# Kernel optimization log

Hardware: AMD Instinct MI355X
Metric: run time of the kernel (lower is better)

## Reference

```python
import jax, jax.numpy as jnp
import numpy as np

B, N, E = 32, 1024, 16384
IN_DIM, HID, OUT = 768, 512, 400
H, F = 2, 200          # gat heads, per-head dim (H*F == OUT)
PAIR = 2 * OUT         # 800
NEG_SLOPE = 0.2


def setup_inputs() -> dict:
    key = jax.random.key(0)
    ks = jax.random.split(key, 20)
    g = lambda k, shp, fan: jax.random.normal(k, shp, jnp.float32) * (1.0 / np.sqrt(fan))
    return {
        "patch_features": jax.random.normal(ks[0], (B, N, IN_DIM), jnp.float32),
        "edges": jax.random.randint(ks[1], (2, E), 0, N, jnp.int32),
        # patch_encoder Mlps: 768 -> 512 (GELU) -> 400
        "enc_w1": g(ks[2], (IN_DIM, HID), IN_DIM), "enc_b1": jnp.zeros((HID,), jnp.float32),
        "enc_w2": g(ks[3], (HID, OUT), HID),      "enc_b2": jnp.zeros((OUT,), jnp.float32),
        # single GATConv: 400 -> 2 heads x 200, concat
        "gat_w": g(ks[4], (OUT, H, F), OUT),
        "att_src": g(ks[5], (H, F), F), "att_dst": g(ks[6], (H, F), F),
        "gat_b": jnp.zeros((H * F,), jnp.float32),
        # predict_head Mlps: 800 -> 800 (GELU) -> 400 (GELU) -> 3
        "h_w1": g(ks[7], (PAIR, PAIR), PAIR),      "h_b1": jnp.zeros((PAIR,), jnp.float32),
        "h_w2": g(ks[8], (PAIR, PAIR // 2), PAIR), "h_b2": jnp.zeros((PAIR // 2,), jnp.float32),
        "h_w3": g(ks[9], (PAIR // 2, 3), PAIR // 2), "h_b3": jnp.zeros((3,), jnp.float32),
    }


def _forward(patch_features, edges, enc_w1, enc_b1, enc_w2, enc_b2,
             gat_w, att_src, att_dst, gat_b,
             h_w1, h_b1, h_w2, h_b2, h_w3, h_b3):
    n = patch_features.shape[1]
    # per-batch patch encoder MLP (dropout inactive at eval)
    enc = jax.nn.gelu(jnp.einsum('bni,ih->bnh', patch_features, enc_w1) + enc_b1)
    enc = jnp.einsum('bnh,ho->bno', enc, enc_w2) + enc_b2   # [B,N,400]

    src0, dst0 = edges[0], edges[1]
    # GATConv adds self-loops
    loops = jnp.arange(n, dtype=edges.dtype)
    src = jnp.concatenate([src0, loops])
    dst = jnp.concatenate([dst0, loops])

    def gat(h):                                   # h: [N,400]
        wh = jnp.einsum('no,ohf->nhf', h, gat_w)  # [N,H,F]
        a_s = jnp.sum(wh * att_src, -1)           # [N,H]
        a_d = jnp.sum(wh * att_dst, -1)
        e = a_s[src] + a_d[dst]                   # [Et,H]
        e = jnp.where(e > 0, e, NEG_SLOPE * e)    # LeakyReLU(0.2)
        m = jax.ops.segment_max(e, dst, num_segments=n)
        ee = jnp.exp(e - m[dst])
        z = jax.ops.segment_sum(ee, dst, num_segments=n)
        coef = ee / z[dst]                        # softmax over incoming edges
        out = jax.ops.segment_sum(coef[:, :, None] * wh[src], dst, num_segments=n)
        return out.reshape(n, H * F) + gat_b      # concat heads + bias

    feat = enc + jax.vmap(gat)(enc)               # residual add per batch

    # pairwise edge gather + predict head
    pair = jnp.concatenate([feat[:, src0], feat[:, dst0]], axis=-1)  # [B,E,800]
    p = jax.nn.gelu(jnp.einsum('bep,pq->beq', pair, h_w1) + h_b1)
    p = jax.nn.gelu(jnp.einsum('beq,qr->ber', p, h_w2) + h_b2)
    pred = jnp.einsum('ber,rs->bes', p, h_w3) + h_b3                 # [B,E,3]
    return feat, pred


def reference(patch_features, edges, enc_w1, enc_b1, enc_w2, enc_b2,
              gat_w, att_src, att_dst, gat_b,
              h_w1, h_b1, h_w2, h_b2, h_w3, h_b3):
    return _forward(patch_features, edges, enc_w1, enc_b1, enc_w2, enc_b2,
                    gat_w, att_src, att_dst, gat_b,
                    h_w1, h_b1, h_w2, h_b2, h_w3, h_b3)
```

## Files before the change

kernel.cpp:

```cpp
#include <hip/hip_runtime.h>
#include <hip/hip_bf16.h>

typedef unsigned short u16;
typedef __attribute__((ext_vector_type(8))) short bf16x8;
typedef __attribute__((ext_vector_type(4))) float f32x4;

#define B_   32
#define N_   1024
#define E_   16384
#define ET_  17408
#define IN_DIM 768
#define HID  512
#define OUT_ 400
#define PAIR_ 800
#define UVW_ 1600
#define FEAT_ELEMS 13107200
#define MAXD 128

__device__ __forceinline__ float u2f(u16 u) {
    union { unsigned int i; float f; } v; v.i = ((unsigned int)u) << 16; return v.f;
}
__device__ __forceinline__ u16 f2u(float f) {
    __hip_bfloat16 h = __float2bfloat16(f);
    return *(u16*)&h;
}
__device__ __forceinline__ unsigned int pack2(float a, float b) {
    return (unsigned int)f2u(a) | ((unsigned int)f2u(b) << 16);
}

__device__ __forceinline__ float gelu_f(float x) {
    const float c = 0.7978845608028654f;
    float u = c * (x + 0.044715f * x * x * x);
    float t = 2.0f / (1.0f + __expf(-2.0f * u)) - 1.0f;
    return 0.5f * x * (1.0f + t);
}

__device__ __forceinline__ void load_lds16(const void* g, void* l) {
    __builtin_amdgcn_global_load_lds(
        (const __attribute__((address_space(1))) void*)g,
        (__attribute__((address_space(3))) void*)l, 16, 0, 0);
}

__global__ void wt_k(const float* __restrict__ W, u16* __restrict__ Wt,
                     int K, int N)
{
    int i = blockIdx.x * 256 + threadIdx.x;
    if (i >= N * K) return;
    int n = i / K, k = i - n * K;
    Wt[i] = f2u(W[(size_t)k * N + n]);
}

__global__ void wtuv_k(const float* __restrict__ W, u16* __restrict__ Wt)
{
    int i = blockIdx.x * 256 + threadIdx.x;
    if (i >= UVW_ * OUT_) return;
    int n = i / OUT_, k = i - n * OUT_;
    int row = (n >= PAIR_) ? OUT_ + k : k;
    int col = (n >= PAIR_) ? n - PAIR_ : n;
    Wt[i] = f2u(W[(size_t)row * PAIR_ + col]);
}

__global__ void f2b_k(const float* __restrict__ X, u16* __restrict__ Y, int n8)
{
    int i = blockIdx.x * 256 + threadIdx.x;
    if (i >= n8) return;
    const float4* p = (const float4*)X + (size_t)i * 2;
    float4 a = p[0], b = p[1];
    uint4 o;
    o.x = pack2(a.x, a.y); o.y = pack2(a.z, a.w);
    o.z = pack2(b.x, b.y); o.w = pack2(b.z, b.w);
    ((uint4*)Y)[i] = o;
}

template<int ASRC, bool DO_GELU, bool HAS_BIAS, bool OUT_F32>
__global__ __launch_bounds__(256)
void mfma_gemm_k(const float* __restrict__ Af, const u16* __restrict__ Ab,
                 const u16* __restrict__ Wt, const float* __restrict__ bias,
                 u16* __restrict__ Cb, float* __restrict__ Cf,
                 int M, int N, int K,
                 const u16* __restrict__ zbuf)
{
    __shared__ __align__(16) u16 As[128 * 64];
    __shared__ __align__(16) u16 Bs[128 * 64];
    const int tid  = threadIdx.x;
    const int gx   = gridDim.x;
    const int nwg  = gx * gridDim.y;
    const int orig = blockIdx.y * gx + blockIdx.x;
    const int qc   = nwg >> 3, rc = nwg & 7;
    const int xcd  = orig & 7, lid = orig >> 3;
    const int wg   = ((xcd < rc) ? xcd * (qc + 1) : rc * (qc + 1) + (xcd - rc) * qc) + lid;
    const int bm   = (wg / gx) * 128;
    const int bn   = (wg % gx) * 128;
    const int wave = tid >> 6;
    const int lane = tid & 63;
    const int wm   = (wave >> 1) * 64;
    const int wn   = (wave & 1) * 64;
    const int lm   = lane & 15;
    const int lq   = lane >> 4;
    const int lb   = lm & 7;
    const int l8 = lane >> 3;
    const int cl = (lane & 7) ^ l8;

    size_t arow[4]; size_t brow[4]; bool bok[4];
    #pragma unroll
    for (int c4 = 0; c4 < 4; ++c4) {
        int rt = wave * 32 + c4 * 8 + l8;
        if (ASRC == 1) arow[c4] = (size_t)(bm + rt) * K;
        int n = bn + rt;
        bok[c4] = (n < N);
        brow[c4] = (size_t)(n < N ? n : 0) * K;
    }
    const int vrow = tid >> 1, vhalf = tid & 1;

    f32x4 acc[4][4] = {};

    for (int k0 = 0; k0 < K; k0 += 64) {
        if (ASRC == 1) {
            int kk = k0 + cl * 8;
            #pragma unroll
            for (int c4 = 0; c4 < 4; ++c4) {
                const u16* ga = (kk < K) ? Ab + arow[c4] + kk : zbuf;
                load_lds16(ga, (char*)As + (wave * 32 + c4 * 8) * 128);
            }
        } else {
            #pragma unroll
            for (int c = 0; c < 4; ++c) {
                int c_log = vhalf * 4 + c;
                int kk = k0 + c_log * 8;
                uint4 wv = make_uint4(0, 0, 0, 0);
                if (kk < K) {
                    const float* p = Af + (size_t)(bm + vrow) * K + kk;
                    float4 v0 = *(const float4*)p;
                    float4 v1 = *(const float4*)(p + 4);
                    wv.x = pack2(v0.x, v0.y); wv.y = pack2(v0.z, v0.w);
                    wv.z = pack2(v1.x, v1.y); wv.w = pack2(v1.z, v1.w);
                }
                int pc = c_log ^ (vrow & 7);
                *(uint4*)((char*)As + vrow * 128 + pc * 16) = wv;
            }
        }
        {
            int kk = k0 + cl * 8;
            #pragma unroll
            for (int c4 = 0; c4 < 4; ++c4) {
                const u16* gb = (bok[c4] && kk < K) ? Wt + brow[c4] + kk : zbuf;
                load_lds16(gb, (char*)Bs + (wave * 32 + c4 * 8) * 128);
            }
        }
        __syncthreads();
        #pragma unroll
        for (int kh = 0; kh < 2; ++kh) {
            bf16x8 af[4], bfr[4];
            #pragma unroll
            for (int t = 0; t < 4; ++t)
                af[t] = *(const bf16x8*)((const char*)As +
                        (wm + t * 16 + lm) * 128 + (((kh * 4 + lq) ^ lb) * 16));
            #pragma unroll
            for (int u = 0; u < 4; ++u)
                bfr[u] = *(const bf16x8*)((const char*)Bs +
                        (wn + u * 16 + lm) * 128 + (((kh * 4 + lq) ^ lb) * 16));
            #pragma unroll
            for (int t = 0; t < 4; ++t)
                #pragma unroll
                for (int u = 0; u < 4; ++u)
                    acc[t][u] = __builtin_amdgcn_mfma_f32_16x16x32_bf16(
                        af[t], bfr[u], acc[t][u], 0, 0, 0);
        }
        __syncthreads();
    }

    #pragma unroll
    for (int u = 0; u < 4; ++u) {
        int col = bn + wn + u * 16 + lm;
        if (col >= N) continue;
        float bv = HAS_BIAS ? bias[col] : 0.f;
        #pragma unroll
        for (int t = 0; t < 4; ++t) {
            #pragma unroll
            for (int r = 0; r < 4; ++r) {
                int rowg = bm + wm + t * 16 + lq * 4 + r;
                float v = acc[t][u][r] + bv;
                if (DO_GELU) v = gelu_f(v);
                if (OUT_F32) {
                    Cf[(size_t)rowg * N + col] = v;
                    if (Cb) Cb[(size_t)rowg * N + col] = f2u(v);
                } else {
                    Cb[(size_t)rowg * N + col] = f2u(v);
                }
            }
        }
    }
}

__global__ __launch_bounds__(256)
void pair_fuse_k(const u16* __restrict__ UV, const float* __restrict__ b1,
                 const int* __restrict__ src0, const int* __restrict__ dst0,
                 u16* __restrict__ p1, int b0, int nrows)
{
    int r  = blockIdx.x * 2 + (threadIdx.x >> 7);
    int c8 = threadIdx.x & 127;
    if (c8 >= 100 || r >= nrows) return;
    int e = r & (E_ - 1);
    int gs, gd;
    if (b0 >= 0) {
        int b = b0 + (r >> 14);
        gs = (b << 10) + src0[e];
        gd = (b << 10) + dst0[e];
    } else {
        gs = src0[e]; gd = dst0[e];
    }
    uint4 qu = *(const uint4*)(UV + (size_t)gs * UVW_ + c8 * 8);
    uint4 qv = *(const uint4*)(UV + (size_t)gd * UVW_ + PAIR_ + c8 * 8);
    float4 bva = *(const float4*)(b1 + c8 * 8);
    float4 bvb = *(const float4*)(b1 + c8 * 8 + 4);
    float bb[8] = {bva.x, bva.y, bva.z, bva.w, bvb.x, bvb.y, bvb.z, bvb.w};
    unsigned int uu[4] = {qu.x, qu.y, qu.z, qu.w};
    unsigned int vv[4] = {qv.x, qv.y, qv.z, qv.w};
    uint4 o; unsigned int* op = (unsigned int*)&o;
    #pragma unroll
    for (int q = 0; q < 4; ++q) {
        float a0 = u2f((u16)(uu[q] & 0xffff)) + u2f((u16)(vv[q] & 0xffff)) + bb[2*q];
        float a1 = u2f((u16)(uu[q] >> 16))    + u2f((u16)(vv[q] >> 16))    + bb[2*q+1];
        op[q] = pack2(gelu_f(a0), gelu_f(a1));
    }
    *(uint4*)(p1 + (size_t)r * PAIR_ + c8 * 8) = o;
}

__global__ __launch_bounds__(256)
void scores_k(const u16* __restrict__ wh, const float* __restrict__ att_s,
              const float* __restrict__ att_d, float* __restrict__ a_s,
              float* __restrict__ a_d)
{
    int n = blockIdx.x * 4 + (threadIdx.x >> 6);
    int lane = threadIdx.x & 63;
    const u16* row = wh + (size_t)n * OUT_;
    float as0 = 0, as1 = 0, ad0 = 0, ad1 = 0;
    for (int f = lane; f < OUT_; f += 64) {
        float v = u2f(row[f]);
        float s = att_s[f];
        float d = att_d[f];
        if (f < 200) { as0 += v * s; ad0 += v * d; }
        else         { as1 += v * s; ad1 += v * d; }
    }
    for (int off = 32; off; off >>= 1) {
        as0 += __shfl_xor(as0, off); as1 += __shfl_xor(as1, off);
        ad0 += __shfl_xor(ad0, off); ad1 += __shfl_xor(ad1, off);
    }
    if (lane == 0) {
        a_s[(size_t)n * 2 + 0] = as0; a_s[(size_t)n * 2 + 1] = as1;
        a_d[(size_t)n * 2 + 0] = ad0; a_d[(size_t)n * 2 + 1] = ad1;
    }
}

__global__ void csr_count_k(const int* __restrict__ edges, int* __restrict__ deg)
{
    int et = blockIdx.x * blockDim.x + threadIdx.x;
    if (et >= ET_) return;
    int dst = (et < E_) ? edges[E_ + et] : (et - E_);
    atomicAdd(&deg[dst], 1);
}

__global__ __launch_bounds__(1024)
void csr_scan_k(const int* __restrict__ deg, int* __restrict__ row_ptr,
                int* __restrict__ cnt)
{
    __shared__ int s[1024];
    int t = threadIdx.x;
    int d = deg[t];
    s[t] = d;
    __syncthreads();
    for (int off = 1; off < 1024; off <<= 1) {
        int v = (t >= off) ? s[t - off] : 0;
        __syncthreads();
        s[t] += v;
        __syncthreads();
    }
    row_ptr[t] = s[t] - d;
    cnt[t] = s[t] - d;
    if (t == 1023) row_ptr[1024] = s[t];
}

__global__ void csr_fill_k(const int* __restrict__ edges, int* __restrict__ cnt,
                           int* __restrict__ col_src)
{
    int et = blockIdx.x * blockDim.x + threadIdx.x;
    if (et >= ET_) return;
    int src, dst;
    if (et < E_) { src = edges[et]; dst = edges[E_ + et]; }
    else         { src = et - E_;  dst = src; }
    int pos = atomicAdd(&cnt[dst], 1);
    col_src[pos] = src;
}

__global__ __launch_bounds__(256)
void gat_k(const u16* __restrict__ wh,
           const float* __restrict__ a_s, const float* __restrict__ a_d,
           const int* __restrict__ row_ptr, const int* __restrict__ col_src,
           const float* __restrict__ gat_b, float* __restrict__ feat,
           u16* __restrict__ featb16)
{
    int gn = blockIdx.x;
    int b = gn >> 10, n = gn & 1023;
    int tid = threadIdx.x;
    __shared__ float s_ee[2][MAXD];
    __shared__ int   s_src[MAXD];
    __shared__ float s_misc[6];
    __shared__ float s_part[4][50][9];
    int start = row_ptr[n];
    int deg = row_ptr[n + 1] - start;

    if (tid < 64) {
        int lane = tid;
        float ad0 = a_d[(size_t)gn * 2 + 0];
        float ad1 = a_d[(size_t)gn * 2 + 1];
        float m0 = -1e30f, m1 = -1e30f;
        for (int j = lane; j < deg; j += 64) {
            int gs = (b << 10) + col_src[start + j];
            float e0 = a_s[(size_t)gs * 2 + 0] + ad0; e0 = (e0 > 0.f) ? e0 : 0.2f * e0;
            float e1 = a_s[(size_t)gs * 2 + 1] + ad1; e1 = (e1 > 0.f) ? e1 : 0.2f * e1;
            if (j < MAXD) { s_ee[0][j] = e0; s_ee[1][j] = e1; s_src[j] = gs; }
            m0 = fmaxf(m0, e0); m1 = fmaxf(m1, e1);
        }
        for (int off = 32; off; off >>= 1) {
            m0 = fmaxf(m0, __shfl_xor(m0, off));
            m1 = fmaxf(m1, __shfl_xor(m1, off));
        }
        float z0 = 0.f, z1 = 0.f;
        for (int j = lane; j < deg; j += 64) {
            float e0, e1;
            if (j < MAXD) { e0 = s_ee[0][j]; e1 = s_ee[1][j]; }
            else {
                int gs = (b << 10) + col_src[start + j];
                e0 = a_s[(size_t)gs * 2 + 0] + ad0; e0 = (e0 > 0.f) ? e0 : 0.2f * e0;
                e1 = a_s[(size_t)gs * 2 + 1] + ad1; e1 = (e1 > 0.f) ? e1 : 0.2f * e1;
            }
            float t0 = __expf(e0 - m0), t1 = __expf(e1 - m1);
            if (j < MAXD) { s_ee[0][j] = t0; s_ee[1][j] = t1; }
            z0 += t0; z1 += t1;
        }
        for (int off = 32; off; off >>= 1) {
            z0 += __shfl_xor(z0, off);
            z1 += __shfl_xor(z1, off);
        }
        if (lane == 0) {
            s_misc[0] = m0; s_misc[1] = m1;
            s_misc[2] = (z0 > 0.f) ? 1.f / z0 : 0.f;
            s_misc[3] = (z1 > 0.f) ? 1.f / z1 : 0.f;
            s_misc[4] = ad0; s_misc[5] = ad1;
        }
    }
    __syncthreads();

    int wv = tid >> 6, ln = tid & 63;
    if (ln < 50) {
        int h = (ln >= 25);
        float m = s_misc[h], ad = s_misc[4 + h];
        float acc[8] = {};
        for (int j = wv; j < deg; j += 4) {
            float w; int gs;
            if (j < MAXD) { w = s_ee[h][j]; gs = s_src[j]; }
            else {
                gs = (b << 10) + col_src[start + j];
                float e = a_s[(size_t)gs * 2 + h] + ad;
                e = (e > 0.f) ? e : 0.2f * e;
                w = __expf(e - m);
            }
            uint4 q = *(const uint4*)(wh + (size_t)gs * OUT_ + ln * 8);
            acc[0] += w * u2f((u16)(q.x & 0xffff));
            acc[1] += w * u2f((u16)(q.x >> 16));
            acc[2] += w * u2f((u16)(q.y & 0xffff));
            acc[3] += w * u2f((u16)(q.y >> 16));
            acc[4] += w * u2f((u16)(q.z & 0xffff));
            acc[5] += w * u2f((u16)(q.z >> 16));
            acc[6] += w * u2f((u16)(q.w & 0xffff));
            acc[7] += w * u2f((u16)(q.w >> 16));
        }
        #pragma unroll
        for (int k = 0; k < 8; ++k) s_part[wv][ln][k] = acc[k];
    }
    __syncthreads();
    if (tid < 50) {
        int h = (tid >= 25);
        float iz = s_misc[2 + h];
        size_t base = (size_t)gn * OUT_ + tid * 8;
        float4 f0 = *(const float4*)(feat + base);
        float4 f1 = *(const float4*)(feat + base + 4);
        float fv[8] = { f0.x, f0.y, f0.z, f0.w, f1.x, f1.y, f1.z, f1.w };
        float o[8];
        #pragma unroll
        for (int k = 0; k < 8; ++k) {
            float s = s_part[0][tid][k] + s_part[1][tid][k] +
                      s_part[2][tid][k] + s_part[3][tid][k];
            o[k] = fv[k] + s * iz + gat_b[tid * 8 + k];
        }
        *(float4*)(feat + base)     = make_float4(o[0], o[1], o[2], o[3]);
        *(float4*)(feat + base + 4) = make_float4(o[4], o[5], o[6], o[7]);
        if (featb16) {
            uint4 bq;
            bq.x = pack2(o[0], o[1]); bq.y = pack2(o[2], o[3]);
            bq.z = pack2(o[4], o[5]); bq.w = pack2(o[6], o[7]);
            *(uint4*)(featb16 + base) = bq;
        }
    }
}

__global__ __launch_bounds__(256)
void head3_k(const u16* __restrict__ p2, const float* __restrict__ w3,
             const float* __restrict__ b3, float* __restrict__ out,
             int row_base, int nrows)
{
    int wv = threadIdx.x >> 6, lane = threadIdx.x & 63;
    float w3r[24];
    if (lane < 50) {
        #pragma unroll
        for (int q = 0; q < 6; ++q) {
            float4 v = *(const float4*)(w3 + lane * 24 + q * 4);
            w3r[q * 4 + 0] = v.x; w3r[q * 4 + 1] = v.y;
            w3r[q * 4 + 2] = v.z; w3r[q * 4 + 3] = v.w;
        }
    }
    int e0 = blockIdx.x * 16 + wv * 4;
    for (int ei = 0; ei < 4; ++ei) {
        int e = e0 + ei;
        if (e >= nrows) break;
        float s0 = 0, s1 = 0, s2 = 0;
        if (lane < 50) {
            uint4 q = *(const uint4*)(p2 + (size_t)e * OUT_ + lane * 8);
            float f[8];
            f[0] = u2f((u16)(q.x & 0xffff)); f[1] = u2f((u16)(q.x >> 16));
            f[2] = u2f((u16)(q.y & 0xffff)); f[3] = u2f((u16)(q.y >> 16));
            f[4] = u2f((u16)(q.z & 0xffff)); f[5] = u2f((u16)(q.z >> 16));
            f[6] = u2f((u16)(q.w & 0xffff)); f[7] = u2f((u16)(q.w >> 16));
            #pragma unroll
            for (int k = 0; k < 8; ++k) {
                s0 += f[k] * w3r[k * 3 + 0];
                s1 += f[k] * w3r[k * 3 + 1];
                s2 += f[k] * w3r[k * 3 + 2];
            }
        }
        for (int off = 32; off; off >>= 1) {
            s0 += __shfl_xor(s0, off);
            s1 += __shfl_xor(s1, off);
            s2 += __shfl_xor(s2, off);
        }
        if (lane == 0) {
            size_t o = (size_t)FEAT_ELEMS + (size_t)(row_base + e) * 3;
            out[o + 0] = s0 + b3[0];
            out[o + 1] = s1 + b3[1];
            out[o + 2] = s2 + b3[2];
        }
    }
}

extern "C" void kernel_launch(void* const* d_in, const int* in_sizes, int n_in,
                              void* d_out, int out_size, void* d_ws, size_t ws_size,
                              hipStream_t stream)
{
    const float* patch  = (const float*)d_in[0];
    const int*   edges  = (const int*)d_in[1];
    const float* enc_w1 = (const float*)d_in[2];
    const float* enc_b1 = (const float*)d_in[3];
    const float* enc_w2 = (const float*)d_in[4];
    const float* enc_b2 = (const float*)d_in[5];
    const float* gat_w  = (const float*)d_in[6];
    const float* att_s  = (const float*)d_in[7];
    const float* att_d  = (const float*)d_in[8];
    const float* gat_b  = (const float*)d_in[9];
    const float* h_w1   = (const float*)d_in[10];
    const float* h_b1   = (const float*)d_in[11];
    const float* h_w2   = (const float*)d_in[12];
    const float* h_b2   = (const float*)d_in[13];
    const float* h_w3   = (const float*)d_in[14];
    const float* h_b3   = (const float*)d_in[15];
    float* out  = (float*)d_out;
    float* feat = out;
    char*  ws   = (char*)d_ws;

    const int* src0 = edges;
    const int* dst0 = edges + E_;

    const size_t R0 = 33554432ull, TAIL = 4194304ull;
    const size_t UVSZ = 104857600ull;
    const size_t PER_B = 39321600ull;
    int CB = 0;
    if (ws_size >= R0 + UVSZ + TAIL + 2 * PER_B)      CB = 2;
    else if (ws_size >= R0 + UVSZ + TAIL + PER_B)     CB = 1;
    const bool big = (CB >= 1);

    u16 *enc1, *whb, *p1, *p2, *featb16, *uv, *w1t, *w2t, *gwt, *uvwt, *hw2t;
    u16 *patchb16, *encb16;
    float *a_s, *a_d; int *deg;
    if (big) {
        enc1    = (u16*)ws;
        featb16 = (u16*)ws;
        whb     = (u16*)(ws + R0);
        uv      = (u16*)(ws + R0);
        encb16  = (u16*)(ws + R0 + 26214400ull);
        p1      = (u16*)(ws + R0 + UVSZ);
        patchb16= (u16*)(ws + R0 + UVSZ);
        p2      = (u16*)(ws + R0 + UVSZ + (size_t)CB * 26214400ull);
        size_t tb = (ws_size - TAIL) & ~(size_t)255;
        w1t  = (u16*)(ws + tb);
        w2t  = (u16*)(ws + tb + 786432);
        gwt  = (u16*)(ws + tb + 1196032);
        uvwt = (u16*)(ws + tb + 1516032);
        hw2t = (u16*)(ws + tb + 2796032);
        a_s  = (float*)(ws + tb + 3436032);
        a_d  = (float*)(ws + tb + 3698176);
        deg  = (int*)(ws + tb + 3960320);
    } else {
        enc1    = (u16*)ws;
        whb     = (u16*)ws;
        p1      = (u16*)ws;
        featb16 = nullptr;
        patchb16= nullptr;
        encb16  = nullptr;
        p2      = (u16*)(ws + 26214400);
        uv      = (u16*)(ws + 39321600);
        w1t  = (u16*)(ws + 42598400);
        w2t  = (u16*)(ws + 43384832);
        gwt  = (u16*)(ws + 43794432);
        uvwt = (u16*)(ws + 44114432);
        hw2t = (u16*)(ws + 45394432);
        a_s  = (float*)(ws + 46034432);
        a_d  = (float*)(ws + 46296576);
        deg  = (int*)(ws + 46558720);
    }
    int* row_ptr = deg + 1024;
    int* cnt     = row_ptr + 1032;
    int* col_src = cnt + 1024;
    u16* zbuf = (u16*)(col_src + 17408);

    hipMemsetAsync(zbuf, 0, 256, stream);

    wt_k<<<(HID * IN_DIM + 255) / 256, 256, 0, stream>>>(enc_w1, w1t, IN_DIM, HID);
    wt_k<<<(OUT_ * HID + 255) / 256, 256, 0, stream>>>(enc_w2, w2t, HID, OUT_);
    wt_k<<<(OUT_ * OUT_ + 255) / 256, 256, 0, stream>>>(gat_w, gwt, OUT_, OUT_);
    wtuv_k<<<(UVW_ * OUT_ + 255) / 256, 256, 0, stream>>>(h_w1, uvwt);
    wt_k<<<(OUT_ * PAIR_ + 255) / 256, 256, 0, stream>>>(h_w2, hw2t, PAIR_, OUT_);

    hipMemsetAsync(deg, 0, 1024 * sizeof(int), stream);
    csr_count_k<<<(ET_ + 255) / 256, 256, 0, stream>>>(edges, deg);
    csr_scan_k<<<1, 1024, 0, stream>>>(deg, row_ptr, cnt);
    csr_fill_k<<<(ET_ + 255) / 256, 256, 0, stream>>>(edges, cnt, col_src);

    if (big) {
        f2b_k<<<(B_ * N_ * IN_DIM / 8 + 255) / 256, 256, 0, stream>>>(
            patch, patchb16, B_ * N_ * IN_DIM / 8);
        mfma_gemm_k<1, true, true, false><<<dim3(HID / 128, (B_ * N_) / 128), 256, 0, stream>>>(
            nullptr, patchb16, w1t, enc_b1, enc1, nullptr, B_ * N_, HID, IN_DIM, zbuf);
        mfma_gemm_k<1, false, true, true><<<dim3((OUT_ + 127) / 128, (B_ * N_) / 128), 256, 0, stream>>>(
            nullptr, enc1, w2t, enc_b2, encb16, feat, B_ * N_, OUT_, HID, zbuf);
        mfma_gemm_k<1, false, false, false><<<dim3((OUT_ + 127) / 128, (B_ * N_) / 128), 256, 0, stream>>>(
            nullptr, encb16, gwt, nullptr, whb, nullptr, B_ * N_, OUT_, OUT_, zbuf);
    } else {
        mfma_gemm_k<0, true, true, false><<<dim3(HID / 128, (B_ * N_) / 128), 256, 0, stream>>>(
            patch, nullptr, w1t, enc_b1, enc1, nullptr, B_ * N_, HID, IN_DIM, zbuf);
        mfma_gemm_k<1, false, true, true><<<dim3((OUT_ + 127) / 128, (B_ * N_) / 128), 256, 0, stream>>>(
            nullptr, enc1, w2t, enc_b2, nullptr, feat, B_ * N_, OUT_, HID, zbuf);
        mfma_gemm_k<0, false, false, false><<<dim3((OUT_ + 127) / 128, (B_ * N_) / 128), 256, 0, stream>>>(
            feat, nullptr, gwt, nullptr, whb, nullptr, B_ * N_, OUT_, OUT_, zbuf);
    }

    scores_k<<<(B_ * N_) / 4, 256, 0, stream>>>(whb, att_s, att_d, a_s, a_d);
    gat_k<<<B_ * N_, 256, 0, stream>>>(whb, a_s, a_d, row_ptr, col_src,
                                       gat_b, feat, featb16);

    if (big) {
        mfma_gemm_k<1, false, false, false><<<dim3((UVW_ + 127) / 128, (B_ * N_) / 128), 256, 0, stream>>>(
            nullptr, featb16, uvwt, nullptr, uv, nullptr, B_ * N_, UVW_, OUT_, zbuf);
        for (int b0 = 0; b0 < B_; b0 += CB) {
            int Mr = CB * E_;
            pair_fuse_k<<<Mr / 2, 256, 0, stream>>>(uv, h_b1, src0, dst0, p1, b0, Mr);
            mfma_gemm_k<1, true, true, false><<<dim3((OUT_ + 127) / 128, Mr / 128), 256, 0, stream>>>(
                nullptr, p1, hw2t, h_b2, p2, nullptr, Mr, OUT_, PAIR_, zbuf);
            head3_k<<<(Mr + 15) / 16, 256, 0, stream>>>(p2, h_w3, h_b3, out,
                                                        b0 * E_, Mr);
        }
    } else {
        for (int b = 0; b < B_; ++b) {
            const float* featb = feat + (size_t)b * N_ * OUT_;
            mfma_gemm_k<0, false, false, false><<<dim3((UVW_ + 127) / 128, N_ / 128), 256, 0, stream>>>(
                featb, nullptr, uvwt, nullptr, uv, nullptr, N_, UVW_, OUT_, zbuf);
            pair_fuse_k<<<E_ / 2, 256, 0, stream>>>(uv, h_b1, src0, dst0, p1, -1, E_);
            mfma_gemm_k<1, true, true, false><<<dim3((OUT_ + 127) / 128, E_ / 128), 256, 0, stream>>>(
                nullptr, p1, hw2t, h_b2, p2, nullptr, E_, OUT_, PAIR_, zbuf);
            head3_k<<<(E_ + 15) / 16, 256, 0, stream>>>(p2, h_w3, h_b3, out,
                                                        b * E_, E_);
        }
    }
}
```

Before: 1.798 ms.

## Fuse final 3-wide head into second head GEMM epilogue via atomics

The second predict-head GEMM now applies GELU, dots each row with the 400x3 final weights in registers, reduces across lanes and atomically adds partial sums into a zeroed output, removing the p2 buffer write/read and the separate head3 kernel. Pair_fuse indexing is repacked so no threads idle (100 of 128 were active before), and the chunk size grows to 4 batches since p2 no longer needs workspace. This adds a large output memset and float atomics across the 4 column tiles, which makes summation order nondeterministic.

```diff
diff --git a/kernel.cpp b/kernel.cpp
--- a/kernel.cpp
+++ b/kernel.cpp
@@ -72,13 +72,15 @@
     ((uint4*)Y)[i] = o;
 }
 
-template<int ASRC, bool DO_GELU, bool HAS_BIAS, bool OUT_F32>
+template<int ASRC, bool DO_GELU, bool HAS_BIAS, bool OUT_F32, bool FUSE_H3>
 __global__ __launch_bounds__(256)
 void mfma_gemm_k(const float* __restrict__ Af, const u16* __restrict__ Ab,
                  const u16* __restrict__ Wt, const float* __restrict__ bias,
                  u16* __restrict__ Cb, float* __restrict__ Cf,
                  int M, int N, int K,
-                 const u16* __restrict__ zbuf)
+                 const u16* __restrict__ zbuf,
+                 const float* __restrict__ w3p, const float* __restrict__ b3p,
+                 float* __restrict__ outp, int row_base)
 {
     __shared__ __align__(16) u16 As[128 * 64];
     __shared__ __align__(16) u16 Bs[128 * 64];
@@ -169,6 +171,48 @@
         __syncthreads();
     }
 
+    if (FUSE_H3) {
+        float w3c[4][3]; float bvv[4];
+        #pragma unroll
+        for (int u = 0; u < 4; ++u) {
+            int col = bn + wn + u * 16 + lm;
+            bool ok = (col < N);
+            bvv[u]    = ok ? bias[col] : 0.f;
+            w3c[u][0] = ok ? w3p[col * 3 + 0] : 0.f;
+            w3c[u][1] = ok ? w3p[col * 3 + 1] : 0.f;
+            w3c[u][2] = ok ? w3p[col * 3 + 2] : 0.f;
+        }
+        #pragma unroll
+        for (int t = 0; t < 4; ++t) {
+            #pragma unroll
+            for (int r = 0; r < 4; ++r) {
+                float s0 = 0.f, s1 = 0.f, s2 = 0.f;
+                #pragma unroll
+                for (int u = 0; u < 4; ++u) {
+                    float v = gelu_f(acc[t][u][r] + bvv[u]);
+                    s0 += v * w3c[u][0];
+                    s1 += v * w3c[u][1];
+                    s2 += v * w3c[u][2];
+                }
+                #pragma unroll
+                for (int off = 8; off; off >>= 1) {
+                    s0 += __shfl_xor(s0, off);
+                    s1 += __shfl_xor(s1, off);
+                    s2 += __shfl_xor(s2, off);
+                }
+                if (lm == 0) {
+                    int rowg = bm + wm + t * 16 + lq * 4 + r;
+                    if (bn == 0 && wn == 0) { s0 += b3p[0]; s1 += b3p[1]; s2 += b3p[2]; }
+                    float* dst = outp + (size_t)(row_base + rowg) * 3;
+                    atomicAdd(dst + 0, s0);
+                    atomicAdd(dst + 1, s1);
+                    atomicAdd(dst + 2, s2);
+                }
+            }
+        }
+        return;
+    }
+
     #pragma unroll
     for (int u = 0; u < 4; ++u) {
         int col = bn + wn + u * 16 + lm;
@@ -197,13 +241,15 @@
                  const int* __restrict__ src0, const int* __restrict__ dst0,
                  u16* __restrict__ p1, int b0, int nrows)
 {
-    int r  = blockIdx.x * 2 + (threadIdx.x >> 7);
-    int c8 = threadIdx.x & 127;
-    if (c8 >= 100 || r >= nrows) return;
+    unsigned idx = blockIdx.x * 256u + threadIdx.x;
+    unsigned total = (unsigned)nrows * 100u;
+    if (idx >= total) return;
+    unsigned r  = (unsigned)(((unsigned long long)idx * 1374389535ull) >> 37);
+    unsigned c8 = idx - r * 100u;
     int e = r & (E_ - 1);
     int gs, gd;
     if (b0 >= 0) {
-        int b = b0 + (r >> 14);
+        int b = b0 + (int)(r >> 14);
         gs = (b << 10) + src0[e];
         gd = (b << 10) + dst0[e];
     } else {
@@ -481,11 +527,11 @@
 
     const size_t R0 = 33554432ull, TAIL = 4194304ull;
     const size_t UVSZ = 104857600ull;
-    const size_t PER_B = 39321600ull;
+    const size_t P1SZ = 26214400ull;
     int CB = 0;
-    if (ws_size >= R0 + UVSZ + TAIL + 2 * PER_B)      CB = 2;
-    else if (ws_size >= R0 + UVSZ + TAIL + PER_B)     CB = 1;
-    const bool big = (CB >= 1);
+    if      (ws_size >= R0 + UVSZ + TAIL + 4 * P1SZ) CB = 4;
+    else if (ws_size >= R0 + UVSZ + TAIL + 2 * P1SZ) CB = 2;
+    const bool big = (CB >= 2);
 
     u16 *enc1, *whb, *p1, *p2, *featb16, *uv, *w1t, *w2t, *gwt, *uvwt, *hw2t;
     u16 *patchb16, *encb16;
@@ -498,7 +544,7 @@
         encb16  = (u16*)(ws + R0 + 26214400ull);
         p1      = (u16*)(ws + R0 + UVSZ);
         patchb16= (u16*)(ws + R0 + UVSZ);
-        p2      = (u16*)(ws + R0 + UVSZ + (size_t)CB * 26214400ull);
+        p2      = nullptr;
         size_t tb = (ws_size - TAIL) & ~(size_t)255;
         w1t  = (u16*)(ws + tb);
         w2t  = (u16*)(ws + tb + 786432);
@@ -532,6 +578,8 @@
     u16* zbuf = (u16*)(col_src + 17408);
 
     hipMemsetAsync(zbuf, 0, 256, stream);
+    if (big)
+        hipMemsetAsync(out + FEAT_ELEMS, 0, (size_t)B_ * E_ * 3 * sizeof(float), stream);
 
     wt_k<<<(HID * IN_DIM + 255) / 256, 256, 0, stream>>>(enc_w1, w1t, IN_DIM, HID);
     wt_k<<<(OUT_ * HID + 255) / 256, 256, 0, stream>>>(enc_w2, w2t, HID, OUT_);
@@ -547,19 +595,25 @@
     if (big) {
         f2b_k<<<(B_ * N_ * IN_DIM / 8 + 255) / 256, 256, 0, stream>>>(
             patch, patchb16, B_ * N_ * IN_DIM / 8);
-        mfma_gemm_k<1, true, true, false><<<dim3(HID / 128, (B_ * N_) / 128), 256, 0, stream>>>(
-            nullptr, patchb16, w1t, enc_b1, enc1, nullptr, B_ * N_, HID, IN_DIM, zbuf);
-        mfma_gemm_k<1, false, true, true><<<dim3((OUT_ + 127) / 128, (B_ * N_) / 128), 256, 0, stream>>>(
-            nullptr, enc1, w2t, enc_b2, encb16, feat, B_ * N_, OUT_, HID, zbuf);
-        mfma_gemm_k<1, false, false, false><<<dim3((OUT_ + 127) / 128, (B_ * N_) / 128), 256, 0, stream>>>(
-            nullptr, encb16, gwt, nullptr, whb, nullptr, B_ * N_, OUT_, OUT_, zbuf);
+        mfma_gemm_k<1, true, true, false, false><<<dim3(HID / 128, (B_ * N_) / 128), 256, 0, stream>>>(
+            nullptr, patchb16, w1t, enc_b1, enc1, nullptr, B_ * N_, HID, IN_DIM, zbuf,
+            nullptr, nullptr, nullptr, 0);
+        mfma_gemm_k<1, false, true, true, false><<<dim3((OUT_ + 127) / 128, (B_ * N_) / 128), 256, 0, stream>>>(
+            nullptr, enc1, w2t, enc_b2, encb16, feat, B_ * N_, OUT_, HID, zbuf,
+            nullptr, nullptr, nullptr, 0);
+        mfma_gemm_k<1, false, false, false, false><<<dim3((OUT_ + 127) / 128, (B_ * N_) / 128), 256, 0, stream>>>(
+            nullptr, encb16, gwt, nullptr, whb, nullptr, B_ * N_, OUT_, OUT_, zbuf,
+            nullptr, nullptr, nullptr, 0);
     } else {
-        mfma_gemm_k<0, true, true, false><<<dim3(HID / 128, (B_ * N_) / 128), 256, 0, stream>>>(
-            patch, nullptr, w1t, enc_b1, enc1, nullptr, B_ * N_, HID, IN_DIM, zbuf);
-        mfma_gemm_k<1, false, true, true><<<dim3((OUT_ + 127) / 128, (B_ * N_) / 128), 256, 0, stream>>>(
-            nullptr, enc1, w2t, enc_b2, nullptr, feat, B_ * N_, OUT_, HID, zbuf);
-        mfma_gemm_k<0, false, false, false><<<dim3((OUT_ + 127) / 128, (B_ * N_) / 128), 256, 0, stream>>>(
-            feat, nullptr, gwt, nullptr, whb, nullptr, B_ * N_, OUT_, OUT_, zbuf);
+        mfma_gemm_k<0, true, true, false, false><<<dim3(HID / 128, (B_ * N_) / 128), 256, 0, stream>>>(
+            patch, nullptr, w1t, enc_b1, enc1, nullptr, B_ * N_, HID, IN_DIM, zbuf,
+            nullptr, nullptr, nullptr, 0);
+        mfma_gemm_k<1, false, true, true, false><<<dim3((OUT_ + 127) / 128, (B_ * N_) / 128), 256, 0, stream>>>(
+            nullptr, enc1, w2t, enc_b2, nullptr, feat, B_ * N_, OUT_, HID, zbuf,
+            nullptr, nullptr, nullptr, 0);
+        mfma_gemm_k<0, false, false, false, false><<<dim3((OUT_ + 127) / 128, (B_ * N_) / 128), 256, 0, stream>>>(
+            feat, nullptr, gwt, nullptr, whb, nullptr, B_ * N_, OUT_, OUT_, zbuf,
+            nullptr, nullptr, nullptr, 0);
     }
 
     scores_k<<<(B_ * N_) / 4, 256, 0, stream>>>(whb, att_s, att_d, a_s, a_d);
@@ -567,24 +621,28 @@
                                        gat_b, feat, featb16);
 
     if (big) {
-        mfma_gemm_k<1, false, false, false><<<dim3((UVW_ + 127) / 128, (B_ * N_) / 128), 256, 0, stream>>>(
-            nullptr, featb16, uvwt, nullptr, uv, nullptr, B_ * N_, UVW_, OUT_, zbuf);
+        mfma_gemm_k<1, false, false, false, false><<<dim3((UVW_ + 127) / 128, (B_ * N_) / 128), 256, 0, stream>>>(
+            nullptr, featb16, uvwt, nullptr, uv, nullptr, B_ * N_, UVW_, OUT_, zbuf,
+            nullptr, nullptr, nullptr, 0);
         for (int b0 = 0; b0 < B_; b0 += CB) {
             int Mr = CB * E_;
-            pair_fuse_k<<<Mr / 2, 256, 0, stream>>>(uv, h_b1, src0, dst0, p1, b0, Mr);
-            mfma_gemm_k<1, true, true, false><<<dim3((OUT_ + 127) / 128, Mr / 128), 256, 0, stream>>>(
-                nullptr, p1, hw2t, h_b2, p2, nullptr, Mr, OUT_, PAIR_, zbuf);
-            head3_k<<<(Mr + 15) / 16, 256, 0, stream>>>(p2, h_w3, h_b3, out,
-                                                        b0 * E_, Mr);
+            pair_fuse_k<<<(Mr * 100 + 255) / 256, 256, 0, stream>>>(
+                uv, h_b1, src0, dst0, p1, b0, Mr);
+            mfma_gemm_k<1, true, true, false, true><<<dim3((OUT_ + 127) / 128, Mr / 128), 256, 0, stream>>>(
+                nullptr, p1, hw2t, h_b2, nullptr, nullptr, Mr, OUT_, PAIR_, zbuf,
+                h_w3, h_b3, out + FEAT_ELEMS, b0 * E_);
         }
     } else {
         for (int b = 0; b < B_; ++b) {
             const float* featb = feat + (size_t)b * N_ * OUT_;
-            mfma_gemm_k<0, false, false, false><<<dim3((UVW_ + 127) / 128, N_ / 128), 256, 0, stream>>>(
-                featb, nullptr, uvwt, nullptr, uv, nullptr, N_, UVW_, OUT_, zbuf);
-            pair_fuse_k<<<E_ / 2, 256, 0, stream>>>(uv, h_b1, src0, dst0, p1, -1, E_);
-            mfma_gemm_k<1, true, true, false><<<dim3((OUT_ + 127) / 128, E_ / 128), 256, 0, stream>>>(
-                nullptr, p1, hw2t, h_b2, p2, nullptr, E_, OUT_, PAIR_, zbuf);
+            mfma_gemm_k<0, false, false, false, false><<<dim3((UVW_ + 127) / 128, N_ / 128), 256, 0, stream>>>(
+                featb, nullptr, uvwt, nullptr, uv, nullptr, N_, UVW_, OUT_, zbuf,
+                nullptr, nullptr, nullptr, 0);
+            pair_fuse_k<<<(E_ * 100 + 255) / 256, 256, 0, stream>>>(
+                uv, h_b1, src0, dst0, p1, -1, E_);
+            mfma_gemm_k<1, true, true, false, false><<<dim3((OUT_ + 127) / 128, E_ / 128), 256, 0, stream>>>(
+                nullptr, p1, hw2t, h_b2, p2, nullptr, E_, OUT_, PAIR_, zbuf,
+                nullptr, nullptr, nullptr, 0);
             head3_k<<<(E_ + 15) / 16, 256, 0, stream>>>(p2, h_w3, h_b3, out,
                                                         b * E_, E_);
         }
```

New measurement: 2.190 ms. 21.8% more time.
